# Performance work log

Hardware: AMD Instinct MI355X
Metric: run time of the kernel (lower is better)

Reference implementation:

```python
import jax, jax.numpy as jnp
import numpy as np


def setup_inputs() -> dict:
    key = jax.random.key(0)
    k1, k2, k3 = jax.random.split(key, 3)
    B, S, E = 4, 4096, 512
    x = jax.random.normal(k1, (B, S, E), dtype=jnp.float32)
    # xavier_uniform for Linear weights; zero biases (per _reset_parameters)
    lim_qkv = float(np.sqrt(6.0 / (E + 3 * E)))
    W_qkv = jax.random.uniform(k2, (3 * E, E), minval=-lim_qkv, maxval=lim_qkv, dtype=jnp.float32)
    b_qkv = jnp.zeros((3 * E,), dtype=jnp.float32)
    lim_out = float(np.sqrt(6.0 / (E + E)))
    W_out = jax.random.uniform(k3, (E, E), minval=-lim_out, maxval=lim_out, dtype=jnp.float32)
    b_out = jnp.zeros((E,), dtype=jnp.float32)
    return {"x": x, "W_qkv": W_qkv, "b_qkv": b_qkv, "W_out": W_out, "b_out": b_out}


def reference(x, W_qkv, b_qkv, W_out, b_out):
    B, S, E = x.shape
    H = 8
    D = E // H
    qkv = x @ W_qkv.T + b_qkv                      # [B,S,3E]
    qkv = qkv.reshape(B, S, H, 3 * D)
    q, k, v = jnp.split(qkv, 3, axis=-1)            # each [B,S,H,D]
    q = jax.nn.sigmoid(q)
    k = jax.nn.sigmoid(k)
    # flow conservation normalizers (sum over seq dim=1, then feature dim=3)
    i = jnp.sum(q * jnp.sum(k, axis=1, keepdims=True), axis=3, keepdims=True)      # [B,S,H,1]
    o = jnp.sum(k * jnp.sum(q, axis=1, keepdims=True), axis=3, keepdims=True)
    i_hat = jnp.sum(q * jnp.sum(k / o, axis=1, keepdims=True), axis=3, keepdims=True)
    o_hat = jnp.sum(k * jnp.sum(q / i, axis=1, keepdims=True), axis=3, keepdims=True)
    # NOTE: faithful to source — matmul batches over (B,S) and contracts the HEAD axis
    vw = v * jax.nn.softmax(o_hat, axis=1)          # [B,S,H,D]
    kv = jnp.einsum('bshd,bshe->bsde', k, vw)       # [B,S,D,D]
    r = jnp.einsum('bshd,bsde->bshe', q / i, kv) * jax.nn.sigmoid(i_hat)  # [B,S,H,D]
    values = r.reshape(B, S, E)
    return values @ W_out.T + b_out
```

## Files before the change

### kernel.cpp

```cpp
#include <hip/hip_runtime.h>
#include <cstdint>
#include <cstddef>

#define B_ 4
#define S_ 4096
#define E_ 512
#define NPOS 16384
#define QKVC 1536
#define K_ 512

typedef unsigned short u16;
typedef u16    u16x8  __attribute__((ext_vector_type(8)));
typedef u16    u16x4  __attribute__((ext_vector_type(4)));
typedef __bf16 bf16x8 __attribute__((ext_vector_type(8)));
typedef float  f32x4  __attribute__((ext_vector_type(4)));

__device__ __forceinline__ u16 f2bf(float f) {
    unsigned u = __builtin_bit_cast(unsigned, f);
    unsigned r = (u + 0x7fffu + ((u >> 16) & 1u)) >> 16;
    return (u16)r;
}
__device__ __forceinline__ float bf2f(u16 u) {
    return __builtin_bit_cast(float, (unsigned)u << 16);
}
__device__ __forceinline__ float rcpf(float x) { return __builtin_amdgcn_rcpf(x); }

__device__ __forceinline__ void async16(const void* g, void* lds) {
    __builtin_amdgcn_global_load_lds(
        (const __attribute__((address_space(1))) unsigned int*)g,
        (__attribute__((address_space(3))) unsigned int*)lds, 16, 0, 0);
}

__global__ void cvt_kernel(const float4* __restrict__ in, u16x4* __restrict__ out, int n4) {
    int i = blockIdx.x * 256 + threadIdx.x;
    if (i < n4) {
        float4 v = in[i];
        u16x4 o;
        o[0] = f2bf(v.x); o[1] = f2bf(v.y); o[2] = f2bf(v.z); o[3] = f2bf(v.w);
        out[i] = o;
    }
}

__device__ __forceinline__ void mfma_step(const u16* AsB, const u16* BsB,
                                          int wm, int wn, int fr, int fkk,
                                          f32x4 (&acc)[4][4]) {
    bf16x8 a[4], b[4];
    #pragma unroll
    for (int i = 0; i < 4; ++i)
        a[i] = *(const bf16x8*)&AsB[(wm + i * 16 + fr) * 32 + fkk];
    #pragma unroll
    for (int j = 0; j < 4; ++j)
        b[j] = *(const bf16x8*)&BsB[(wn + j * 16 + fr) * 32 + fkk];
    __builtin_amdgcn_s_setprio(1);
    #pragma unroll
    for (int i = 0; i < 4; ++i)
        #pragma unroll
        for (int j = 0; j < 4; ++j)
            acc[i][j] = __builtin_amdgcn_mfma_f32_16x16x32_bf16(a[i], b[j], acc[i][j], 0, 0, 0);
    __builtin_amdgcn_s_setprio(0);
}

#define GEMM_PIPELINE(NT)                                                     \
    {                                                                          \
        STAGE(0, 0);                                                           \
        STAGE(1, 1);                                                           \
        asm volatile("s_waitcnt vmcnt(4)" ::: "memory");                       \
        __builtin_amdgcn_s_barrier();                                          \
        __builtin_amdgcn_sched_barrier(0);                                     \
        int cb = 0, sb = 1;                                                    \
        for (int t = 0; t < (NT) - 2; ++t) {                                   \
            sb = (sb == 2) ? 0 : sb + 1;                                       \
            STAGE(t + 2, sb);                                                  \
            mfma_step(As[cb], Bs[cb], wm, wn, fr, fkk, acc);                   \
            asm volatile("s_waitcnt vmcnt(4)" ::: "memory");                   \
            __builtin_amdgcn_s_barrier();                                      \
            __builtin_amdgcn_sched_barrier(0);                                 \
            cb = (cb == 2) ? 0 : cb + 1;                                       \
        }                                                                      \
        mfma_step(As[cb], Bs[cb], wm, wn, fr, fkk, acc);                       \
        asm volatile("s_waitcnt vmcnt(0)" ::: "memory");                       \
        __builtin_amdgcn_s_barrier();                                          \
        __builtin_amdgcn_sched_barrier(0);                                     \
        cb = (cb == 2) ? 0 : cb + 1;                                           \
        mfma_step(As[cb], Bs[cb], wm, wn, fr, fkk, acc);                       \
    }

__global__ __launch_bounds__(256) void gemm_qkv(
        const u16* __restrict__ A, const u16* __restrict__ Bw,
        const float* __restrict__ bias,
        u16* __restrict__ Qb, u16* __restrict__ Kb, u16* __restrict__ Vb,
        float* __restrict__ sumq, float* __restrict__ sumk,
        int K) {
    __shared__ u16 As[3][128 * 32];
    __shared__ u16 Bs[3][128 * 32];
    const int tid  = threadIdx.x;
    const int wave = tid >> 6, lane = tid & 63;
    const int m0 = blockIdx.y * 128, n0 = blockIdx.x * 128;
    const int wm = (wave & 1) * 64, wn = (wave >> 1) * 64;

    const int srow = wave * 16 + (lane >> 2);
    const int cgs  = (lane & 3) ^ ((lane >> 2) & 3) ^ ((lane >> 4) & 3);
    const u16* Ap = A  + (size_t)(m0 + srow) * K + cgs * 8;
    const u16* Bp = Bw + (size_t)(n0 + srow) * K + cgs * 8;
    const int woff = wave * 512;
    const size_t rstep = (size_t)64 * K;

    f32x4 acc[4][4] = {};
    const int fr  = lane & 15;
    const int fkk = (((lane >> 4) ^ (fr & 3) ^ ((fr >> 2) & 3))) * 8;

    #define STAGE(t, buf)                                             \
        async16(Ap + (t) * 32,         &As[buf][woff]);               \
        async16(Ap + (t) * 32 + rstep, &As[buf][woff + 2048]);        \
        async16(Bp + (t) * 32,         &Bs[buf][woff]);               \
        async16(Bp + (t) * 32 + rstep, &Bs[buf][woff + 2048]);

    const int nt = K >> 5;
    GEMM_PIPELINE(nt)
    #undef STAGE

    const int cn = lane & 15, rb = (lane >> 4) * 4;
    const int cg   = (n0 + wn) >> 6;
    const int type = cg % 3;
    const int hb   = cg / 3;
    u16* dst = (type == 0) ? Qb : (type == 1) ? Kb : Vb;
    const bool sg = (type < 2);
    float colsum[4] = {};
    #pragma unroll
    for (int i = 0; i < 4; ++i) {
        int mbase = m0 + wm + i * 16 + rb;
        #pragma unroll
        for (int j = 0; j < 4; ++j) {
            int ccol = j * 16 + cn;
            float bv = bias[n0 + wn + ccol];
            int outcol = hb * 64 + ccol;
            f32x4 av = acc[i][j];
            #pragma unroll
            for (int r = 0; r < 4; ++r) {
                float v = av[r] + bv;
                if (sg) { v = 1.f / (1.f + __expf(-v)); colsum[j] += v; }
                dst[(size_t)(mbase + r) * 512 + outcol] = f2bf(v);
            }
        }
    }
    if (sg) {
        float* sdst = (type == 0) ? sumq : sumk;
        const int b = m0 >> 12;
        #pragma unroll
        for (int j = 0; j < 4; ++j) {
            float s = colsum[j];
            s += __shfl_xor(s, 16);
            s += __shfl_xor(s, 32);
            if (lane < 16)
                atomicAdd(&sdst[b * 512 + hb * 64 + j * 16 + cn], s);
        }
    }
}

__global__ __launch_bounds__(256) void gemm_out(
        const u16* __restrict__ A, const u16* __restrict__ Bw,
        const float* __restrict__ bias, float* __restrict__ C,
        int N, int K) {
    __shared__ u16 As[3][128 * 32];
    __shared__ u16 Bs[3][128 * 32];
    const int tid  = threadIdx.x;
    const int wave = tid >> 6, lane = tid & 63;
    const int m0 = blockIdx.y * 128, n0 = blockIdx.x * 128;
    const int wm = (wave & 1) * 64, wn = (wave >> 1) * 64;
    const int srow = wave * 16 + (lane >> 2);
    const int cgs  = (lane & 3) ^ ((lane >> 2) & 3) ^ ((lane >> 4) & 3);
    const u16* Ap = A  + (size_t)(m0 + srow) * K + cgs * 8;
    const u16* Bp = Bw + (size_t)(n0 + srow) * K + cgs * 8;
    const int woff = wave * 512;
    const size_t rstep = (size_t)64 * K;
    f32x4 acc[4][4] = {};
    const int fr  = lane & 15;
    const int fkk = (((lane >> 4) ^ (fr & 3) ^ ((fr >> 2) & 3))) * 8;

    #define STAGE(t, buf)                                             \
        async16(Ap + (t) * 32,         &As[buf][woff]);               \
        async16(Ap + (t) * 32 + rstep, &As[buf][woff + 2048]);        \
        async16(Bp + (t) * 32,         &Bs[buf][woff]);               \
        async16(Bp + (t) * 32 + rstep, &Bs[buf][woff + 2048]);

    const int nt = K >> 5;
    GEMM_PIPELINE(nt)
    #undef STAGE

    const int cn = lane & 15, rb = (lane >> 4) * 4;
    #pragma unroll
    for (int i = 0; i < 4; ++i) {
        int mbase = m0 + wm + i * 16 + rb;
        #pragma unroll
        for (int j = 0; j < 4; ++j) {
            int nn = n0 + wn + j * 16 + cn;
            float bv = bias[nn];
            f32x4 av = acc[i][j];
            #pragma unroll
            for (int r = 0; r < 4; ++r)
                C[(size_t)(mbase + r) * N + nn] = av[r] + bv;
        }
    }
}

__global__ __launch_bounds__(256) void fused_io(const u16* __restrict__ Qg, const u16* __restrict__ Kg,
                                                const float* __restrict__ sumq, const float* __restrict__ sumk,
                                                float* __restrict__ iv,
                                                float* __restrict__ sumqi, float* __restrict__ sumko) {
    int b = blockIdx.x, sc = blockIdx.y;
    int w = threadIdx.x >> 6, lane = threadIdx.x & 63;
    float skL[8], sqL[8];
    #pragma unroll
    for (int j = 0; j < 8; ++j) {
        skL[j] = sumk[b * 512 + lane * 8 + j];
        sqL[j] = sumq[b * 512 + lane * 8 + j];
    }
    float aqi[8] = {}, ako[8] = {};
    int p0 = b * S_ + sc * 32 + w * 8;
    for (int it = 0; it < 8; ++it) {
        int p = p0 + it;
        size_t off = (size_t)p * 512 + lane * 8;
        u16x8 q8 = *(const u16x8*)(Qg + off);
        u16x8 k8 = *(const u16x8*)(Kg + off);
        float qf[8], kf[8];
        #pragma unroll
        for (int j = 0; j < 8; ++j) { qf[j] = bf2f(q8[j]); kf[j] = bf2f(k8[j]); }
        float di = 0.f, dox = 0.f;
        #pragma unroll
        for (int j = 0; j < 8; ++j) { di += qf[j] * skL[j]; dox += kf[j] * sqL[j]; }
        di  += __shfl_xor(di, 1);  di  += __shfl_xor(di, 2);  di  += __shfl_xor(di, 4);
        dox += __shfl_xor(dox, 1); dox += __shfl_xor(dox, 2); dox += __shfl_xor(dox, 4);
        if ((lane & 7) == 0) iv[(size_t)p * 8 + (lane >> 3)] = di;
        float ri = rcpf(di), ro = rcpf(dox);
        #pragma unroll
        for (int j = 0; j < 8; ++j) { aqi[j] += qf[j] * ri; ako[j] += kf[j] * ro; }
    }
    __shared__ float red[4][1024];
    #pragma unroll
    for (int j = 0; j < 8; ++j) {
        red[w][lane * 8 + j]       = aqi[j];
        red[w][512 + lane * 8 + j] = ako[j];
    }
    __syncthreads();
    int t = threadIdx.x;
    #pragma unroll
    for (int rr = 0; rr < 4; ++rr) {
        int slot = rr * 256 + t;
        float s = red[0][slot] + red[1][slot] + red[2][slot] + red[3][slot];
        float* dst = (slot < 512) ? &sumqi[b * 512 + slot] : &sumko[b * 512 + (slot - 512)];
        atomicAdd(dst, s);
    }
}

__global__ __launch_bounds__(256) void io2_kernel(const u16* __restrict__ Qg, const u16* __restrict__ Kg,
                                                  const float* __restrict__ sumqi, const float* __restrict__ sumko,
                                                  const float* __restrict__ iv,
                                                  float* __restrict__ rowsc, float* __restrict__ wexp,
                                                  float* __restrict__ sm) {
    int b = blockIdx.x, sc = blockIdx.y;
    int w = threadIdx.x >> 6, lane = threadIdx.x & 63;
    float skoL[8], sqiL[8];
    #pragma unroll
    for (int j = 0; j < 8; ++j) {
        skoL[j] = sumko[b * 512 + lane * 8 + j];
        sqiL[j] = sumqi[b * 512 + lane * 8 + j];
    }
    float smacc = 0.f;
    int p0 = b * S_ + sc * 32 + w * 8;
    for (int it = 0; it < 8; ++it) {
        int p = p0 + it;
        size_t off = (size_t)p * 512 + lane * 8;
        u16x8 q8 = *(const u16x8*)(Qg + off);
        u16x8 k8 = *(const u16x8*)(Kg + off);
        float dih = 0.f, doh = 0.f;
        #pragma unroll
        for (int j = 0; j < 8; ++j) {
            dih += bf2f(q8[j]) * skoL[j];
            doh += bf2f(k8[j]) * sqiL[j];
        }
        dih += __shfl_xor(dih, 1); dih += __shfl_xor(dih, 2); dih += __shfl_xor(dih, 4);
        doh += __shfl_xor(doh, 1); doh += __shfl_xor(doh, 2); doh += __shfl_xor(doh, 4);
        if ((lane & 7) == 0) {
            int h = lane >> 3;
            float sig = 1.f / (1.f + __expf(-dih));
            rowsc[(size_t)p * 8 + h] = sig * rcpf(iv[(size_t)p * 8 + h]);
            float we = __expf(fminf(doh, 80.f));
            wexp[(size_t)p * 8 + h] = we;
            smacc += we;
        }
    }
    __shared__ float sr[4][8];
    if ((lane & 7) == 0) sr[w][lane >> 3] = smacc;
    __syncthreads();
    if (threadIdx.x < 8)
        atomicAdd(&sm[b * 8 + threadIdx.x],
                  sr[0][threadIdx.x] + sr[1][threadIdx.x] + sr[2][threadIdx.x] + sr[3][threadIdx.x]);
}

__global__ __launch_bounds__(256) void finalize_kernel(
        const u16* __restrict__ Qg, const u16* __restrict__ Kg, const u16* __restrict__ Vg,
        const float* __restrict__ rowsc, const float* __restrict__ wexp, const float* __restrict__ sm,
        u16* __restrict__ Rg) {
    __shared__ float Ml[4][2][8][9];
    __shared__ float vw[4][2][8][68];
    int w = threadIdx.x >> 6, lane = threadIdx.x & 63;
    int p0 = (blockIdx.x * 4 + w) * 2;
    int b = p0 >> 12;

    {
        int pl = (lane >> 3) & 1, hh = lane & 7, quad = lane >> 4;
        const u16* qa = Qg + (size_t)(p0 + pl) * 512 + hh * 64 + quad * 8;
        const u16* ka = Kg + (size_t)(p0 + pl) * 512 + hh * 64 + quad * 8;
        bf16x8 a0 = __builtin_bit_cast(bf16x8, *(const u16x8*)qa);
        bf16x8 a1 = __builtin_bit_cast(bf16x8, *(const u16x8*)(qa + 32));
        bf16x8 b0 = __builtin_bit_cast(bf16x8, *(const u16x8*)ka);
        bf16x8 b1 = __builtin_bit_cast(bf16x8, *(const u16x8*)(ka + 32));
        f32x4 accm = {0.f, 0.f, 0.f, 0.f};
        accm = __builtin_amdgcn_mfma_f32_16x16x32_bf16(a0, b0, accm, 0, 0, 0);
        accm = __builtin_amdgcn_mfma_f32_16x16x32_bf16(a1, b1, accm, 0, 0, 0);
        if (((lane >> 5) & 1) == ((lane >> 3) & 1)) {
            int plm = lane >> 5, hr = ((lane >> 4) & 1) * 4, h2 = lane & 7;
            #pragma unroll
            for (int r = 0; r < 4; ++r) Ml[w][plm][hr + r][h2] = accm[r];
        }
    }
    {
        int hv = lane >> 3, e0 = (lane & 7) * 8;
        float invsm = rcpf(sm[b * 8 + hv]);
        #pragma unroll
        for (int pl = 0; pl < 2; ++pl) {
            u16x8 v8 = *(const u16x8*)(Vg + (size_t)(p0 + pl) * 512 + lane * 8);
            float wgt = wexp[(size_t)(p0 + pl) * 8 + hv] * invsm;
            f32x4 x0, x1;
            #pragma unroll
            for (int j = 0; j < 4; ++j) { x0[j] = bf2f(v8[j]) * wgt; x1[j] = bf2f(v8[4 + j]) * wgt; }
            *(f32x4*)&vw[w][pl][hv][e0]     = x0;
            *(f32x4*)&vw[w][pl][hv][e0 + 4] = x1;
        }
    }
    __syncthreads();
    {
        int pl = lane >> 5, idx = lane & 31, h = idx >> 2, eq = (idx & 3) * 16;
        float out[16] = {};
        #pragma unroll
        for (int h2 = 0; h2 < 8; ++h2) {
            float m = Ml[w][pl][h][h2];
            #pragma unroll
            for (int c = 0; c < 4; ++c) {
                f32x4 vv = *(const f32x4*)&vw[w][pl][h2][eq + c * 4];
                #pragma unroll
                for (int j = 0; j < 4; ++j) out[c * 4 + j] += m * vv[j];
            }
        }
        float rs = rowsc[(size_t)(p0 + pl) * 8 + h];
        u16x8 o0, o1;
        #pragma unroll
        for (int j = 0; j < 8; ++j) { o0[j] = f2bf(out[j] * rs); o1[j] = f2bf(out[8 + j] * rs); }
        u16* dst = Rg + (size_t)(p0 + pl) * 512 + h * 64 + eq;
        *(u16x8*)dst       = o0;
        *(u16x8*)(dst + 8) = o1;
    }
}

extern "C" void kernel_launch(void* const* d_in, const int* in_sizes, int n_in,
                              void* d_out, int out_size, void* d_ws, size_t ws_size,
                              hipStream_t stream) {
    const float* x    = (const float*)d_in[0];
    const float* Wqkv = (const float*)d_in[1];
    const float* bqkv = (const float*)d_in[2];
    const float* Wout = (const float*)d_in[3];
    const float* bout = (const float*)d_in[4];
    float* out = (float*)d_out;
    char* ws = (char*)d_ws;

    constexpr size_t SZ_XBF  = (size_t)NPOS * E_ * 2;
    constexpr size_t SZ_WQBF = (size_t)QKVC * E_ * 2;
    constexpr size_t SZ_WOBF = (size_t)E_ * E_ * 2;
    constexpr size_t SZ_QKVB = (size_t)NPOS * E_ * 2;
    constexpr size_t SZ_SUM  = (size_t)B_ * 512 * 4;
    constexpr size_t SZ_V8   = (size_t)NPOS * 8 * 4;

    size_t off = 0;
    u16*   xbf   = (u16*)(ws + off);   off += SZ_XBF;
    u16*   wqbf  = (u16*)(ws + off);   off += SZ_WQBF;
    u16*   wobf  = (u16*)(ws + off);   off += SZ_WOBF;
    u16*   Qb    = (u16*)(ws + off);   off += SZ_QKVB;
    u16*   Kb    = (u16*)(ws + off);   off += SZ_QKVB;
    u16*   Vb    = (u16*)(ws + off);   off += SZ_QKVB;
    char*  zbase = ws + off;
    float* sumq  = (float*)(ws + off); off += SZ_SUM;
    float* sumk  = (float*)(ws + off); off += SZ_SUM;
    float* sumqi = (float*)(ws + off); off += SZ_SUM;
    float* sumko = (float*)(ws + off); off += SZ_SUM;
    float* sm    = (float*)(ws + off); off += 256;
    size_t zlen  = (char*)(ws + off) - zbase;
    float* iv    = (float*)(ws + off); off += SZ_V8;
    float* rowsc = (float*)(ws + off); off += SZ_V8;
    float* wexp  = (float*)(ws + off); off += SZ_V8;
    u16*   rbf   = xbf;

    hipMemsetAsync(zbase, 0, zlen, stream);

    cvt_kernel<<<(NPOS * E_ / 4) / 256, 256, 0, stream>>>((const float4*)x, (u16x4*)xbf, NPOS * E_ / 4);
    cvt_kernel<<<(QKVC * E_ / 4) / 256, 256, 0, stream>>>((const float4*)Wqkv, (u16x4*)wqbf, QKVC * E_ / 4);
    cvt_kernel<<<(E_ * E_ / 4) / 256, 256, 0, stream>>>((const float4*)Wout, (u16x4*)wobf, E_ * E_ / 4);

    gemm_qkv<<<dim3(QKVC / 128, NPOS / 128), 256, 0, stream>>>(xbf, wqbf, bqkv, Qb, Kb, Vb, sumq, sumk, K_);

    fused_io<<<dim3(B_, 128), 256, 0, stream>>>(Qb, Kb, sumq, sumk, iv, sumqi, sumko);
    io2_kernel<<<dim3(B_, 128), 256, 0, stream>>>(Qb, Kb, sumqi, sumko, iv, rowsc, wexp, sm);
    finalize_kernel<<<NPOS / 8, 256, 0, stream>>>(Qb, Kb, Vb, rowsc, wexp, sm, rbf);

    gemm_out<<<dim3(E_ / 128, NPOS / 128), 256, 0, stream>>>(rbf, wobf, bout, out, E_, K_);
}
```

Before: 192.0 us.

## Enlarge QKV GEMM tile to 256x256 with 512 threads and 4-stage pipeline

After: 210.4 us. 1.1x slower.

```diff
diff --git a/kernel.cpp b/kernel.cpp
--- a/kernel.cpp
+++ b/kernel.cpp
@@ -41,82 +41,69 @@
     }
 }
 
-__device__ __forceinline__ void mfma_step(const u16* AsB, const u16* BsB,
-                                          int wm, int wn, int fr, int fkk,
-                                          f32x4 (&acc)[4][4]) {
-    bf16x8 a[4], b[4];
-    #pragma unroll
-    for (int i = 0; i < 4; ++i)
-        a[i] = *(const bf16x8*)&AsB[(wm + i * 16 + fr) * 32 + fkk];
-    #pragma unroll
-    for (int j = 0; j < 4; ++j)
-        b[j] = *(const bf16x8*)&BsB[(wn + j * 16 + fr) * 32 + fkk];
-    __builtin_amdgcn_s_setprio(1);
-    #pragma unroll
-    for (int i = 0; i < 4; ++i)
-        #pragma unroll
-        for (int j = 0; j < 4; ++j)
-            acc[i][j] = __builtin_amdgcn_mfma_f32_16x16x32_bf16(a[i], b[j], acc[i][j], 0, 0, 0);
-    __builtin_amdgcn_s_setprio(0);
-}
-
-#define GEMM_PIPELINE(NT)                                                     \
-    {                                                                          \
-        STAGE(0, 0);                                                           \
-        STAGE(1, 1);                                                           \
-        asm volatile("s_waitcnt vmcnt(4)" ::: "memory");                       \
-        __builtin_amdgcn_s_barrier();                                          \
-        __builtin_amdgcn_sched_barrier(0);                                     \
-        int cb = 0, sb = 1;                                                    \
-        for (int t = 0; t < (NT) - 2; ++t) {                                   \
-            sb = (sb == 2) ? 0 : sb + 1;                                       \
-            STAGE(t + 2, sb);                                                  \
-            mfma_step(As[cb], Bs[cb], wm, wn, fr, fkk, acc);                   \
-            asm volatile("s_waitcnt vmcnt(4)" ::: "memory");                   \
-            __builtin_amdgcn_s_barrier();                                      \
-            __builtin_amdgcn_sched_barrier(0);                                 \
-            cb = (cb == 2) ? 0 : cb + 1;                                       \
-        }                                                                      \
-        mfma_step(As[cb], Bs[cb], wm, wn, fr, fkk, acc);                       \
-        asm volatile("s_waitcnt vmcnt(0)" ::: "memory");                       \
-        __builtin_amdgcn_s_barrier();                                          \
-        __builtin_amdgcn_sched_barrier(0);                                     \
-        cb = (cb == 2) ? 0 : cb + 1;                                           \
-        mfma_step(As[cb], Bs[cb], wm, wn, fr, fkk, acc);                       \
-    }
-
-__global__ __launch_bounds__(256) void gemm_qkv(
+__global__ __launch_bounds__(512) void gemm_qkv(
         const u16* __restrict__ A, const u16* __restrict__ Bw,
         const float* __restrict__ bias,
         u16* __restrict__ Qb, u16* __restrict__ Kb, u16* __restrict__ Vb,
         float* __restrict__ sumq, float* __restrict__ sumk,
         int K) {
-    __shared__ u16 As[3][128 * 32];
-    __shared__ u16 Bs[3][128 * 32];
+    __shared__ u16 As[4][256 * 32];
+    __shared__ u16 Bs[4][256 * 32];
     const int tid  = threadIdx.x;
     const int wave = tid >> 6, lane = tid & 63;
-    const int m0 = blockIdx.y * 128, n0 = blockIdx.x * 128;
-    const int wm = (wave & 1) * 64, wn = (wave >> 1) * 64;
-
-    const int srow = wave * 16 + (lane >> 2);
-    const int cgs  = (lane & 3) ^ ((lane >> 2) & 3) ^ ((lane >> 4) & 3);
-    const u16* Ap = A  + (size_t)(m0 + srow) * K + cgs * 8;
-    const u16* Bp = Bw + (size_t)(n0 + srow) * K + cgs * 8;
+    const int m0 = blockIdx.y * 256, n0 = blockIdx.x * 256;
+    const int wm = (wave >> 2) * 128;
+    const int wn = (wave & 3) * 64;
+
+    const int srow = tid >> 2;
+    const int scol = (tid & 3) * 8;
+    const u16* Ap = A  + (size_t)(m0 + srow) * K + scol;
+    const u16* Bp = Bw + (size_t)(n0 + srow) * K + scol;
     const int woff = wave * 512;
-    const size_t rstep = (size_t)64 * K;
-
-    f32x4 acc[4][4] = {};
-    const int fr  = lane & 15;
-    const int fkk = (((lane >> 4) ^ (fr & 3) ^ ((fr >> 2) & 3))) * 8;
-
-    #define STAGE(t, buf)                                             \
-        async16(Ap + (t) * 32,         &As[buf][woff]);               \
-        async16(Ap + (t) * 32 + rstep, &As[buf][woff + 2048]);        \
-        async16(Bp + (t) * 32,         &Bs[buf][woff]);               \
-        async16(Bp + (t) * 32 + rstep, &Bs[buf][woff + 2048]);
-
-    const int nt = K >> 5;
-    GEMM_PIPELINE(nt)
+    const size_t rstep = (size_t)128 * K;
+
+    f32x4 acc[8][4] = {};
+    const int fr = lane & 15, fk = (lane >> 4) * 8;
+
+    #define STAGE(t)                                                     \
+        { int bb = (t) & 3;                                              \
+          async16(Ap + (t) * 32,         &As[bb][woff]);                 \
+          async16(Ap + (t) * 32 + rstep, &As[bb][woff + 4096]);          \
+          async16(Bp + (t) * 32,         &Bs[bb][woff]);                 \
+          async16(Bp + (t) * 32 + rstep, &Bs[bb][woff + 4096]); }
+
+    const int NT = K >> 5;
+    STAGE(0); STAGE(1); STAGE(2);
+    asm volatile("s_waitcnt vmcnt(8)" ::: "memory");
+    __builtin_amdgcn_s_barrier();
+    __builtin_amdgcn_sched_barrier(0);
+
+    for (int t = 0; t < NT; ++t) {
+        const u16* Ab = As[t & 3];
+        const u16* Bb = Bs[t & 3];
+        if (t + 3 < NT) STAGE(t + 3);
+        bf16x8 b[4], a[8];
+        #pragma unroll
+        for (int j = 0; j < 4; ++j)
+            b[j] = *(const bf16x8*)&Bb[(wn + j * 16 + fr) * 32 + fk];
+        #pragma unroll
+        for (int i = 0; i < 8; ++i)
+            a[i] = *(const bf16x8*)&Ab[(wm + i * 16 + fr) * 32 + fk];
+        __builtin_amdgcn_s_setprio(1);
+        #pragma unroll
+        for (int i = 0; i < 8; ++i)
+            #pragma unroll
+            for (int j = 0; j < 4; ++j)
+                acc[i][j] = __builtin_amdgcn_mfma_f32_16x16x32_bf16(a[i], b[j], acc[i][j], 0, 0, 0);
+        __builtin_amdgcn_s_setprio(0);
+        if (t < NT - 1) {
+            if (t < NT - 3)       asm volatile("s_waitcnt vmcnt(8)" ::: "memory");
+            else if (t == NT - 3) asm volatile("s_waitcnt vmcnt(4)" ::: "memory");
+            else                  asm volatile("s_waitcnt vmcnt(0)" ::: "memory");
+            __builtin_amdgcn_s_barrier();
+            __builtin_amdgcn_sched_barrier(0);
+        }
+    }
     #undef STAGE
 
     const int cn = lane & 15, rb = (lane >> 4) * 4;
@@ -127,7 +114,7 @@
     const bool sg = (type < 2);
     float colsum[4] = {};
     #pragma unroll
-    for (int i = 0; i < 4; ++i) {
+    for (int i = 0; i < 8; ++i) {
         int mbase = m0 + wm + i * 16 + rb;
         #pragma unroll
         for (int j = 0; j < 4; ++j) {
@@ -155,6 +142,25 @@
                 atomicAdd(&sdst[b * 512 + hb * 64 + j * 16 + cn], s);
         }
     }
+}
+
+__device__ __forceinline__ void mfma_step(const u16* AsB, const u16* BsB,
+                                          int wm, int wn, int fr, int fkk,
+                                          f32x4 (&acc)[4][4]) {
+    bf16x8 a[4], b[4];
+    #pragma unroll
+    for (int i = 0; i < 4; ++i)
+        a[i] = *(const bf16x8*)&AsB[(wm + i * 16 + fr) * 32 + fkk];
+    #pragma unroll
+    for (int j = 0; j < 4; ++j)
+        b[j] = *(const bf16x8*)&BsB[(wn + j * 16 + fr) * 32 + fkk];
+    __builtin_amdgcn_s_setprio(1);
+    #pragma unroll
+    for (int i = 0; i < 4; ++i)
+        #pragma unroll
+        for (int j = 0; j < 4; ++j)
+            acc[i][j] = __builtin_amdgcn_mfma_f32_16x16x32_bf16(a[i], b[j], acc[i][j], 0, 0, 0);
+    __builtin_amdgcn_s_setprio(0);
 }
 
 __global__ __launch_bounds__(256) void gemm_out(
@@ -184,7 +190,27 @@
         async16(Bp + (t) * 32 + rstep, &Bs[buf][woff + 2048]);
 
     const int nt = K >> 5;
-    GEMM_PIPELINE(nt)
+    STAGE(0, 0);
+    STAGE(1, 1);
+    asm volatile("s_waitcnt vmcnt(4)" ::: "memory");
+    __builtin_amdgcn_s_barrier();
+    __builtin_amdgcn_sched_barrier(0);
+    int cb = 0, sb = 1;
+    for (int t = 0; t < nt - 2; ++t) {
+        sb = (sb == 2) ? 0 : sb + 1;
+        STAGE(t + 2, sb);
+        mfma_step(As[cb], Bs[cb], wm, wn, fr, fkk, acc);
+        asm volatile("s_waitcnt vmcnt(4)" ::: "memory");
+        __builtin_amdgcn_s_barrier();
+        __builtin_amdgcn_sched_barrier(0);
+        cb = (cb == 2) ? 0 : cb + 1;
+    }
+    mfma_step(As[cb], Bs[cb], wm, wn, fr, fkk, acc);
+    asm volatile("s_waitcnt vmcnt(0)" ::: "memory");
+    __builtin_amdgcn_s_barrier();
+    __builtin_amdgcn_sched_barrier(0);
+    cb = (cb == 2) ? 0 : cb + 1;
+    mfma_step(As[cb], Bs[cb], wm, wn, fr, fkk, acc);
     #undef STAGE
 
     const int cn = lane & 15, rb = (lane >> 4) * 4;
@@ -405,7 +431,7 @@
     cvt_kernel<<<(QKVC * E_ / 4) / 256, 256, 0, stream>>>((const float4*)Wqkv, (u16x4*)wqbf, QKVC * E_ / 4);
     cvt_kernel<<<(E_ * E_ / 4) / 256, 256, 0, stream>>>((const float4*)Wout, (u16x4*)wobf, E_ * E_ / 4);
 
-    gemm_qkv<<<dim3(QKVC / 128, NPOS / 128), 256, 0, stream>>>(xbf, wqbf, bqkv, Qb, Kb, Vb, sumq, sumk, K_);
+    gemm_qkv<<<dim3(QKVC / 256, NPOS / 256), 512, 0, stream>>>(xbf, wqbf, bqkv, Qb, Kb, Vb, sumq, sumk, K_);
 
     fused_io<<<dim3(B_, 128), 256, 0, stream>>>(Qb, Kb, sumq, sumk, iv, sumqi, sumko);
     io2_kernel<<<dim3(B_, 128), 256, 0, stream>>>(Qb, Kb, sumqi, sumko, iv, rowsc, wexp, sm);
```
